# Performance work log

Hardware: AMD Instinct MI355X
Metric: run time of the kernel (lower is better)

## Reference

```python
import jax, jax.numpy as jnp
import numpy as np

N_NODES = 50000
N_EDGES = 800000
D_IN = 128
D_HID = 128
D_OUT = 128


def gcn_conv(x, W, b, src, dst, n_nodes):
    """PyG GCNConv: sym-normalized A+I aggregation, then bias.
    messages flow src -> dst; self-loops handled analytically."""
    h = x @ W  # [N, F_out]
    ones = jnp.ones(src.shape[0], dtype=h.dtype)
    deg = jax.ops.segment_sum(ones, dst, num_segments=n_nodes) + 1.0  # +1 self-loop
    dinv = jax.lax.rsqrt(deg)  # deg^-1/2
    norm = dinv[src] * dinv[dst]  # [E]
    agg = jax.ops.segment_sum(h[src] * norm[:, None], dst, num_segments=n_nodes)
    out = agg + h * (dinv * dinv)[:, None]  # self-loop term: dinv[i]^2 * h[i]
    return out + b


def setup_inputs() -> dict:
    key = jax.random.key(0)
    ks = jax.random.split(key, 12)
    x = jax.random.normal(ks[0], (N_NODES, D_IN), dtype=jnp.float32)
    edge_index = jax.random.randint(ks[1], (2, N_EDGES), 0, N_NODES, dtype=jnp.int64)

    def lin(k, fi, fo):
        s = 1.0 / np.sqrt(fi)
        return jax.random.uniform(k, (fi, fo), jnp.float32, -s, s)

    return {
        "x": x,
        "edge_index": edge_index,
        "W1": lin(ks[2], D_IN, D_HID), "b1": jnp.zeros((D_HID,), jnp.float32),
        "W2": lin(ks[3], D_HID, D_HID), "b2": jnp.zeros((D_HID,), jnp.float32),
        "W3": lin(ks[4], D_HID, D_OUT), "b3": jnp.zeros((D_OUT,), jnp.float32),
        "Wm1": lin(ks[5], 2 * D_HID, D_HID), "bm1": jnp.zeros((D_HID,), jnp.float32),
        "Wm2": lin(ks[6], D_HID, D_HID), "bm2": jnp.zeros((D_HID,), jnp.float32),
    }


def reference(x, edge_index, W1, b1, W2, b2, W3, b3, Wm1, bm1, Wm2, bm2):
    src, dst = edge_index[0], edge_index[1]
    n = x.shape[0]
    h = jax.nn.relu(gcn_conv(x, W1, b1, src, dst, n))
    h = jax.nn.relu(gcn_conv(h, W2, b2, src, dst, n))
    h = gcn_conv(h, W3, b3, src, dst, n)
    # edge head: gather node pairs, concat, 2-layer MLP
    ef = jnp.concatenate([h[src], h[dst]], axis=1)  # [E, 2*hidden]
    es = jax.nn.relu(ef @ Wm1 + bm1) @ Wm2 + bm2  # [E, hidden]
    return jnp.squeeze(es)
```

## Files before the change

kernel.cpp:

```cpp
#include <hip/hip_runtime.h>
#include <stdint.h>

typedef __attribute__((ext_vector_type(8))) short bf16x8;
typedef __attribute__((ext_vector_type(4))) float f32x4;

static __device__ __forceinline__ unsigned short f2b(float f) {
    unsigned int u = __float_as_uint(f);
    unsigned int r = u + 0x7fffu + ((u >> 16) & 1u);
    return (unsigned short)(r >> 16);
}
static __device__ __forceinline__ float b2f(unsigned short u) {
    return __uint_as_float((unsigned int)u << 16);
}
static __device__ __forceinline__ f32x4 b2f4(ushort4 u) {
    f32x4 r;
    r[0] = b2f(u.x); r[1] = b2f(u.y); r[2] = b2f(u.z); r[3] = b2f(u.w);
    return r;
}


__global__ void count_deg(const int* __restrict__ dst, int E, int* __restrict__ counts) {
    int e = blockIdx.x * 256 + threadIdx.x;
    if (e < E) atomicAdd(&counts[dst[e]], 1);
}

__global__ void scan_s1(const int* __restrict__ counts, int N,
                        int* __restrict__ rowstart, float* __restrict__ dinv,
                        int* __restrict__ psum) {
    __shared__ int wsum[16];
    int tid = threadIdx.x, wave = tid >> 6, lane = tid & 63;
    int i = blockIdx.x * 1024 + tid;
    int c = (i < N) ? counts[i] : 0;
    int x = c;
    #pragma unroll
    for (int off = 1; off < 64; off <<= 1) {
        int v = __shfl_up(x, off);
        if (lane >= off) x += v;
    }
    if (lane == 63) wsum[wave] = x;
    __syncthreads();
    int pre = 0, tot = 0;
    #pragma unroll
    for (int w = 0; w < 16; ++w) {
        int s = wsum[w];
        tot += s;
        if (w < wave) pre += s;
    }
    if (i < N) {
        rowstart[i] = pre + x - c;
        dinv[i] = rsqrtf((float)c + 1.0f);
    }
    if (tid == 0) psum[blockIdx.x] = tot;
}

__global__ void scan_s2(int* __restrict__ psum, int nchunk,
                        int* __restrict__ rowstart, int N) {
    __shared__ int wsum[16];
    int tid = threadIdx.x, wave = tid >> 6, lane = tid & 63;
    int v = (tid < nchunk) ? psum[tid] : 0;
    int x = v;
    #pragma unroll
    for (int off = 1; off < 64; off <<= 1) {
        int s = __shfl_up(x, off);
        if (lane >= off) x += s;
    }
    if (lane == 63) wsum[wave] = x;
    __syncthreads();
    int pre = 0, tot = 0;
    #pragma unroll
    for (int w = 0; w < 16; ++w) {
        int s = wsum[w];
        tot += s;
        if (w < wave) pre += s;
    }
    if (tid < nchunk) psum[tid] = pre + x - v;
    if (tid == 0) rowstart[N] = tot;
}

__global__ void scan_s3(int* __restrict__ rowstart, const int* __restrict__ psum,
                        int N, int* __restrict__ cursor) {
    int i = blockIdx.x * 1024 + threadIdx.x;
    if (i < N) {
        int r = rowstart[i] + psum[blockIdx.x];
        rowstart[i] = r;
        cursor[i] = r;
    }
}

__global__ void fill_csr(const int* __restrict__ src, const int* __restrict__ dst, int E,
                         int* __restrict__ cursor, int* __restrict__ csr_src,
                         int* __restrict__ csr_dst, int* __restrict__ csr_eid) {
    int e = blockIdx.x * 256 + threadIdx.x;
    if (e < E) {
        int d = dst[e];
        int p = atomicAdd(&cursor[d], 1);
        csr_src[p] = src[e];
        csr_dst[p] = d;
        csr_eid[p] = e;
    }
}


template <int IN_F32>
__global__ __launch_bounds__(256) void node_mfma(const void* __restrict__ inp,
                                                 const float* __restrict__ W,
                                                 unsigned short* __restrict__ outb, int N) {
    __shared__ __align__(16) unsigned short hl[64][136];
    int tid = threadIdx.x;
    int wid = tid >> 6, lane = tid & 63;
    int lg = lane >> 4, l15 = lane & 15;
    int tilebase = blockIdx.x * 64;

    bf16x8 a[2][4];
    #pragma unroll
    for (int mt = 0; mt < 2; ++mt) {
        int col = wid * 32 + mt * 16 + l15;
        #pragma unroll
        for (int kk = 0; kk < 4; ++kk) {
            bf16x8 af;
            #pragma unroll
            for (int ee = 0; ee < 8; ++ee)
                af[ee] = (short)f2b(W[(size_t)(kk * 32 + lg * 8 + ee) * 128 + col]);
            a[mt][kk] = af;
        }
    }

    #pragma unroll
    for (int p = 0; p < 4; ++p) {
        int idx = p * 256 + tid;
        int r = idx >> 4, ci = idx & 15;
        int row = tilebase + r;
        if (row >= N) row = N - 1;
        if (IN_F32) {
            const float* ip = (const float*)inp + (size_t)row * 128 + ci * 8;
            f32x4 x0 = *(const f32x4*)ip;
            f32x4 x1 = *(const f32x4*)(ip + 4);
            uint4 v;
            v.x = (unsigned int)f2b(x0[0]) | ((unsigned int)f2b(x0[1]) << 16);
            v.y = (unsigned int)f2b(x0[2]) | ((unsigned int)f2b(x0[3]) << 16);
            v.z = (unsigned int)f2b(x1[0]) | ((unsigned int)f2b(x1[1]) << 16);
            v.w = (unsigned int)f2b(x1[2]) | ((unsigned int)f2b(x1[3]) << 16);
            *(uint4*)&hl[r][ci * 8] = v;
        } else {
            *(uint4*)&hl[r][ci * 8] =
                *(const uint4*)((const unsigned short*)inp + (size_t)row * 128 + ci * 8);
        }
    }
    __syncthreads();

    f32x4 acc[2][4];
    #pragma unroll
    for (int mt = 0; mt < 2; ++mt)
        #pragma unroll
        for (int nt = 0; nt < 4; ++nt) acc[mt][nt] = (f32x4){0.f, 0.f, 0.f, 0.f};
    #pragma unroll
    for (int kk = 0; kk < 4; ++kk) {
        #pragma unroll
        for (int nt = 0; nt < 4; ++nt) {
            bf16x8 b = *(const bf16x8*)&hl[nt * 16 + l15][kk * 32 + lg * 8];
            acc[0][nt] = __builtin_amdgcn_mfma_f32_16x16x32_bf16(a[0][kk], b, acc[0][nt], 0, 0, 0);
            acc[1][nt] = __builtin_amdgcn_mfma_f32_16x16x32_bf16(a[1][kk], b, acc[1][nt], 0, 0, 0);
        }
    }
    #pragma unroll
    for (int mt = 0; mt < 2; ++mt) {
        int j = wid * 32 + mt * 16 + lg * 4;
        #pragma unroll
        for (int nt = 0; nt < 4; ++nt) {
            int node = tilebase + nt * 16 + l15;
            if (node < N) {
                unsigned int u0 = (unsigned int)f2b(acc[mt][nt][0]) | ((unsigned int)f2b(acc[mt][nt][1]) << 16);
                unsigned int u1 = (unsigned int)f2b(acc[mt][nt][2]) | ((unsigned int)f2b(acc[mt][nt][3]) << 16);
                *(uint2*)(outb + (size_t)node * 128 + j) = make_uint2(u0, u1);
            }
        }
    }
}


template <int RELU>
__global__ __launch_bounds__(256) void aggregate(
        const unsigned short* __restrict__ tb, const int* __restrict__ rowstart,
        const int* __restrict__ csr_src, const float* __restrict__ dinv,
        const float* __restrict__ bias, unsigned short* __restrict__ hb, int N) {
    int tid = threadIdx.x;
    int node = blockIdx.x * 8 + (tid >> 5);
    if (node >= N) return;
    int c = (tid & 31) * 4;
    float di = dinv[node];
    f32x4 self = b2f4(*(const ushort4*)(tb + (size_t)node * 128 + c));
    f32x4 acc = *(const f32x4*)(bias + c) + (di * di) * self;
    int rs = rowstart[node], re = rowstart[node + 1];
    int e = rs;
    for (; e + 3 < re; e += 4) {
        int s0 = csr_src[e], s1 = csr_src[e + 1];
        int s2 = csr_src[e + 2], s3 = csr_src[e + 3];
        float n0 = dinv[s0], n1 = dinv[s1], n2 = dinv[s2], n3 = dinv[s3];
        ushort4 r0 = *(const ushort4*)(tb + (size_t)s0 * 128 + c);
        ushort4 r1 = *(const ushort4*)(tb + (size_t)s1 * 128 + c);
        ushort4 r2 = *(const ushort4*)(tb + (size_t)s2 * 128 + c);
        ushort4 r3 = *(const ushort4*)(tb + (size_t)s3 * 128 + c);
        acc += (n0 * di) * b2f4(r0);
        acc += (n1 * di) * b2f4(r1);
        acc += (n2 * di) * b2f4(r2);
        acc += (n3 * di) * b2f4(r3);
    }
    for (; e < re; ++e) {
        int s0 = csr_src[e];
        acc += (dinv[s0] * di) * b2f4(*(const ushort4*)(tb + (size_t)s0 * 128 + c));
    }
    if (RELU) {
        #pragma unroll
        for (int j = 0; j < 4; ++j) acc[j] = fmaxf(acc[j], 0.f);
    }
    unsigned int u0 = (unsigned int)f2b(acc[0]) | ((unsigned int)f2b(acc[1]) << 16);
    unsigned int u1 = (unsigned int)f2b(acc[2]) | ((unsigned int)f2b(acc[3]) << 16);
    *(uint2*)(hb + (size_t)node * 128 + c) = make_uint2(u0, u1);
}


__global__ __launch_bounds__(256) void uv_gemm(const unsigned short* __restrict__ h3b,
                                               const float* __restrict__ Wm1,
                                               unsigned short* __restrict__ uvb, int N) {
    __shared__ __align__(16) unsigned short hl[64][136];
    int tid = threadIdx.x;
    int wid = tid >> 6, lane = tid & 63;
    int lg = lane >> 4, l15 = lane & 15;
    int tilebase = blockIdx.x * 64;

    bf16x8 a[4][4];
    #pragma unroll
    for (int mt = 0; mt < 4; ++mt) {
        int jc = wid * 64 + mt * 16 + l15;
        int koff = (jc >> 7) * 128;
        int col = jc & 127;
        #pragma unroll
        for (int kk = 0; kk < 4; ++kk) {
            bf16x8 af;
            #pragma unroll
            for (int ee = 0; ee < 8; ++ee)
                af[ee] = (short)f2b(Wm1[(size_t)(koff + kk * 32 + lg * 8 + ee) * 128 + col]);
            a[mt][kk] = af;
        }
    }

    #pragma unroll
    for (int p = 0; p < 4; ++p) {
        int idx = p * 256 + tid;
        int r = idx >> 4, ci = idx & 15;
        int row = tilebase + r;
        if (row >= N) row = N - 1;
        uint4 v = *(const uint4*)(h3b + (size_t)row * 128 + ci * 8);
        *(uint4*)&hl[r][ci * 8] = v;
    }
    __syncthreads();

    f32x4 acc[4][4];
    #pragma unroll
    for (int mt = 0; mt < 4; ++mt)
        #pragma unroll
        for (int nt = 0; nt < 4; ++nt) acc[mt][nt] = (f32x4){0.f, 0.f, 0.f, 0.f};
    #pragma unroll
    for (int kk = 0; kk < 4; ++kk) {
        #pragma unroll
        for (int nt = 0; nt < 4; ++nt) {
            bf16x8 b = *(const bf16x8*)&hl[nt * 16 + l15][kk * 32 + lg * 8];
            #pragma unroll
            for (int mt = 0; mt < 4; ++mt)
                acc[mt][nt] = __builtin_amdgcn_mfma_f32_16x16x32_bf16(a[mt][kk], b, acc[mt][nt], 0, 0, 0);
        }
    }
    #pragma unroll
    for (int mt = 0; mt < 4; ++mt) {
        int jc = wid * 64 + mt * 16 + lg * 4;
        #pragma unroll
        for (int nt = 0; nt < 4; ++nt) {
            int node = tilebase + nt * 16 + l15;
            if (node < N) {
                unsigned int u0 = (unsigned int)f2b(acc[mt][nt][0]) | ((unsigned int)f2b(acc[mt][nt][1]) << 16);
                unsigned int u1 = (unsigned int)f2b(acc[mt][nt][2]) | ((unsigned int)f2b(acc[mt][nt][3]) << 16);
                *(uint2*)(uvb + (size_t)node * 256 + jc) = make_uint2(u0, u1);
            }
        }
    }
}


__global__ __launch_bounds__(256, 4) void edge_head3(
        const unsigned short* __restrict__ uvb, const int* __restrict__ csr_src,
        const int* __restrict__ csr_dst, const int* __restrict__ csr_eid,
        const float* __restrict__ bm1, const float* __restrict__ Wm2,
        const float* __restrict__ bm2, float* __restrict__ out, int E, int ntiles) {
    __shared__ __align__(16) unsigned short zl[64][136];
    __shared__ int eid_l[64];
    int tid = threadIdx.x;
    int wid = tid >> 6, lane = tid & 63;
    int lg = lane >> 4, l15 = lane & 15;
    int es = tid >> 4;
    int ci = tid & 15;
    int c0 = ci * 8;

    bf16x8 a2[2][4];
    float b2v[2][4];
    #pragma unroll
    for (int mt = 0; mt < 2; ++mt) {
        int m = wid * 32 + mt * 16 + l15;
        #pragma unroll
        for (int kk = 0; kk < 4; ++kk) {
            bf16x8 af;
            #pragma unroll
            for (int ee = 0; ee < 8; ++ee)
                af[ee] = (short)f2b(Wm2[(size_t)(kk * 32 + lg * 8 + ee) * 128 + m]);
            a2[mt][kk] = af;
        }
        #pragma unroll
        for (int r = 0; r < 4; ++r)
            b2v[mt][r] = bm2[wid * 32 + mt * 16 + lg * 4 + r];
    }
    float bm1v[8];
    #pragma unroll
    for (int j = 0; j < 8; ++j) bm1v[j] = bm1[c0 + j];

    for (int tile = blockIdx.x; tile < ntiles; tile += gridDim.x) {
        __syncthreads();
        #pragma unroll
        for (int p = 0; p < 4; ++p) {
            int slot = tile * 64 + p * 16 + es;
            int cs = (slot < E) ? slot : (E - 1);
            int s = csr_src[cs], d = csr_dst[cs];
            if (ci == 0) eid_l[p * 16 + es] = (slot < E) ? csr_eid[cs] : -1;
            uint4 uu = *(const uint4*)(uvb + (size_t)s * 256 + c0);
            uint4 vv = *(const uint4*)(uvb + (size_t)d * 256 + 128 + c0);
            unsigned int w[4];
            {
                float z0 = fmaxf(b2f((unsigned short)(uu.x)) + b2f((unsigned short)(vv.x)) + bm1v[0], 0.f);
                float z1 = fmaxf(b2f((unsigned short)(uu.x >> 16)) + b2f((unsigned short)(vv.x >> 16)) + bm1v[1], 0.f);
                float z2 = fmaxf(b2f((unsigned short)(uu.y)) + b2f((unsigned short)(vv.y)) + bm1v[2], 0.f);
                float z3 = fmaxf(b2f((unsigned short)(uu.y >> 16)) + b2f((unsigned short)(vv.y >> 16)) + bm1v[3], 0.f);
                float z4 = fmaxf(b2f((unsigned short)(uu.z)) + b2f((unsigned short)(vv.z)) + bm1v[4], 0.f);
                float z5 = fmaxf(b2f((unsigned short)(uu.z >> 16)) + b2f((unsigned short)(vv.z >> 16)) + bm1v[5], 0.f);
                float z6 = fmaxf(b2f((unsigned short)(uu.w)) + b2f((unsigned short)(vv.w)) + bm1v[6], 0.f);
                float z7 = fmaxf(b2f((unsigned short)(uu.w >> 16)) + b2f((unsigned short)(vv.w >> 16)) + bm1v[7], 0.f);
                w[0] = (unsigned int)f2b(z0) | ((unsigned int)f2b(z1) << 16);
                w[1] = (unsigned int)f2b(z2) | ((unsigned int)f2b(z3) << 16);
                w[2] = (unsigned int)f2b(z4) | ((unsigned int)f2b(z5) << 16);
                w[3] = (unsigned int)f2b(z6) | ((unsigned int)f2b(z7) << 16);
            }
            *(uint4*)&zl[p * 16 + es][c0] = make_uint4(w[0], w[1], w[2], w[3]);
        }
        __syncthreads();

        f32x4 c2[2][4];
        #pragma unroll
        for (int mt = 0; mt < 2; ++mt)
            #pragma unroll
            for (int nt = 0; nt < 4; ++nt) c2[mt][nt] = (f32x4){0.f, 0.f, 0.f, 0.f};
        #pragma unroll
        for (int kk = 0; kk < 4; ++kk) {
            #pragma unroll
            for (int nt = 0; nt < 4; ++nt) {
                bf16x8 b = *(const bf16x8*)&zl[nt * 16 + l15][kk * 32 + lg * 8];
                c2[0][nt] = __builtin_amdgcn_mfma_f32_16x16x32_bf16(a2[0][kk], b, c2[0][nt], 0, 0, 0);
                c2[1][nt] = __builtin_amdgcn_mfma_f32_16x16x32_bf16(a2[1][kk], b, c2[1][nt], 0, 0, 0);
            }
        }
        #pragma unroll
        for (int mt = 0; mt < 2; ++mt) {
            #pragma unroll
            for (int nt = 0; nt < 4; ++nt) {
                int eg = eid_l[nt * 16 + l15];
                if (eg >= 0) {
                    f32x4 o;
                    #pragma unroll
                    for (int r = 0; r < 4; ++r) o[r] = c2[mt][nt][r] + b2v[mt][r];
                    *(f32x4*)(out + (size_t)eg * 128 + wid * 32 + mt * 16 + lg * 4) = o;
                }
            }
        }
    }
}


extern "C" void kernel_launch(void* const* d_in, const int* in_sizes, int n_in,
                              void* d_out, int out_size, void* d_ws, size_t ws_size,
                              hipStream_t stream) {
    const float* x  = (const float*)d_in[0];
    const int*   ei = (const int*)d_in[1];
    const float* W1 = (const float*)d_in[2];
    const float* b1 = (const float*)d_in[3];
    const float* W2 = (const float*)d_in[4];
    const float* b2 = (const float*)d_in[5];
    const float* W3 = (const float*)d_in[6];
    const float* b3 = (const float*)d_in[7];
    const float* Wm1 = (const float*)d_in[8];
    const float* bm1 = (const float*)d_in[9];
    const float* Wm2 = (const float*)d_in[10];
    const float* bm2 = (const float*)d_in[11];
    float* out = (float*)d_out;

    const int N = in_sizes[0] / 128;
    const int E = in_sizes[1] / 2;
    const int* src = ei;
    const int* dstp = ei + E;

    uintptr_t base = (uintptr_t)d_ws;
    auto alloc = [&](size_t bytes) -> void* {
        uintptr_t p = base;
        base += (bytes + 255) & ~(uintptr_t)255;
        return (void*)p;
    };
    int*   counts   = (int*)alloc((size_t)(N + 1) * 4);
    int*   rowstart = (int*)alloc((size_t)(N + 1) * 4);
    int*   cursor   = (int*)alloc((size_t)N * 4);
    float* dinv     = (float*)alloc((size_t)N * 4);
    int*   psum     = (int*)alloc(4096);
    int*   csr_s    = (int*)alloc((size_t)E * 4);
    int*   csr_d    = (int*)alloc((size_t)E * 4);
    int*   csr_e    = (int*)alloc((size_t)E * 4);
    unsigned short* tb  = (unsigned short*)alloc((size_t)N * 128 * 2);
    unsigned short* hb  = (unsigned short*)alloc((size_t)N * 128 * 2);
    unsigned short* uvb = (unsigned short*)alloc((size_t)N * 256 * 2);
    (void)ws_size; (void)n_in; (void)out_size;

    hipMemsetAsync(counts, 0, (size_t)(N + 1) * 4, stream);

    int egrid = (E + 255) / 256;
    int nchunk = (N + 1023) / 1024;
    count_deg<<<egrid, 256, 0, stream>>>(dstp, E, counts);
    scan_s1<<<nchunk, 1024, 0, stream>>>(counts, N, rowstart, dinv, psum);
    scan_s2<<<1, 1024, 0, stream>>>(psum, nchunk, rowstart, N);
    scan_s3<<<nchunk, 1024, 0, stream>>>(rowstart, psum, N, cursor);
    fill_csr<<<egrid, 256, 0, stream>>>(src, dstp, E, cursor, csr_s, csr_d, csr_e);

    int ggrid = (N + 63) / 64;
    int agrid = (N + 7) / 8;
    node_mfma<1><<<ggrid, 256, 0, stream>>>(x, W1, tb, N);
    aggregate<1><<<agrid, 256, 0, stream>>>(tb, rowstart, csr_s, dinv, b1, hb, N);
    node_mfma<0><<<ggrid, 256, 0, stream>>>(hb, W2, tb, N);
    aggregate<1><<<agrid, 256, 0, stream>>>(tb, rowstart, csr_s, dinv, b2, hb, N);
    node_mfma<0><<<ggrid, 256, 0, stream>>>(hb, W3, tb, N);
    aggregate<0><<<agrid, 256, 0, stream>>>(tb, rowstart, csr_s, dinv, b3, hb, N);

    uv_gemm<<<ggrid, 256, 0, stream>>>(hb, Wm1, uvb, N);

    int ntiles = (E + 63) / 64;
    int hgrid = ntiles < 2048 ? ntiles : 2048;
    edge_head3<<<hgrid, 256, 0, stream>>>(uvb, csr_s, csr_d, csr_e, bm1, Wm2, bm2, out, E, ntiles);
}
```

Baseline: 431.2 us.

## Precompute edge norms into CSR and software-pipeline edge head gathers

The CSR fill now stores each edge's symmetric normalization next to its source index as an int2. This removes the random dinv gather from all three aggregation passes, and the aggregation loop is unrolled to 8 edges. The edge head kernel prefetches the next tile's source-row gathers and indices into registers while the current tile's MFMA runs. Its grid and occupancy are also reduced to 768 blocks at 3 waves per SIMD. The cost is more register pressure and fewer resident blocks in the edge head.

```diff
diff --git a/kernel.cpp b/kernel.cpp
--- a/kernel.cpp
+++ b/kernel.cpp
@@ -88,13 +88,15 @@
 }
 
 __global__ void fill_csr(const int* __restrict__ src, const int* __restrict__ dst, int E,
-                         int* __restrict__ cursor, int* __restrict__ csr_src,
-                         int* __restrict__ csr_dst, int* __restrict__ csr_eid) {
+                         int* __restrict__ cursor, const float* __restrict__ dinv,
+                         int2* __restrict__ csr_sn, int* __restrict__ csr_dst,
+                         int* __restrict__ csr_eid) {
     int e = blockIdx.x * 256 + threadIdx.x;
     if (e < E) {
-        int d = dst[e];
+        int d = dst[e], s = src[e];
         int p = atomicAdd(&cursor[d], 1);
-        csr_src[p] = src[e];
+        float nrm = dinv[s] * dinv[d];
+        csr_sn[p] = make_int2(s, __float_as_int(nrm));
         csr_dst[p] = d;
         csr_eid[p] = e;
     }
@@ -181,7 +183,7 @@
 template <int RELU>
 __global__ __launch_bounds__(256) void aggregate(
         const unsigned short* __restrict__ tb, const int* __restrict__ rowstart,
-        const int* __restrict__ csr_src, const float* __restrict__ dinv,
+        const int2* __restrict__ csr_sn, const float* __restrict__ dinv,
         const float* __restrict__ bias, unsigned short* __restrict__ hb, int N) {
     int tid = threadIdx.x;
     int node = blockIdx.x * 8 + (tid >> 5);
@@ -190,24 +192,41 @@
     float di = dinv[node];
     f32x4 self = b2f4(*(const ushort4*)(tb + (size_t)node * 128 + c));
     f32x4 acc = *(const f32x4*)(bias + c) + (di * di) * self;
-    int rs = rowstart[node], re = rowstart[node + 1];
-    int e = rs;
+    int e = rowstart[node], re = rowstart[node + 1];
+    for (; e + 7 < re; e += 8) {
+        int2 p0 = csr_sn[e + 0], p1 = csr_sn[e + 1], p2 = csr_sn[e + 2], p3 = csr_sn[e + 3];
+        int2 p4 = csr_sn[e + 4], p5 = csr_sn[e + 5], p6 = csr_sn[e + 6], p7 = csr_sn[e + 7];
+        ushort4 r0 = *(const ushort4*)(tb + (size_t)p0.x * 128 + c);
+        ushort4 r1 = *(const ushort4*)(tb + (size_t)p1.x * 128 + c);
+        ushort4 r2 = *(const ushort4*)(tb + (size_t)p2.x * 128 + c);
+        ushort4 r3 = *(const ushort4*)(tb + (size_t)p3.x * 128 + c);
+        ushort4 r4 = *(const ushort4*)(tb + (size_t)p4.x * 128 + c);
+        ushort4 r5 = *(const ushort4*)(tb + (size_t)p5.x * 128 + c);
+        ushort4 r6 = *(const ushort4*)(tb + (size_t)p6.x * 128 + c);
+        ushort4 r7 = *(const ushort4*)(tb + (size_t)p7.x * 128 + c);
+        acc += __int_as_float(p0.y) * b2f4(r0);
+        acc += __int_as_float(p1.y) * b2f4(r1);
+        acc += __int_as_float(p2.y) * b2f4(r2);
+        acc += __int_as_float(p3.y) * b2f4(r3);
+        acc += __int_as_float(p4.y) * b2f4(r4);
+        acc += __int_as_float(p5.y) * b2f4(r5);
+        acc += __int_as_float(p6.y) * b2f4(r6);
+        acc += __int_as_float(p7.y) * b2f4(r7);
+    }
     for (; e + 3 < re; e += 4) {
-        int s0 = csr_src[e], s1 = csr_src[e + 1];
-        int s2 = csr_src[e + 2], s3 = csr_src[e + 3];
-        float n0 = dinv[s0], n1 = dinv[s1], n2 = dinv[s2], n3 = dinv[s3];
-        ushort4 r0 = *(const ushort4*)(tb + (size_t)s0 * 128 + c);
-        ushort4 r1 = *(const ushort4*)(tb + (size_t)s1 * 128 + c);
-        ushort4 r2 = *(const ushort4*)(tb + (size_t)s2 * 128 + c);
-        ushort4 r3 = *(const ushort4*)(tb + (size_t)s3 * 128 + c);
-        acc += (n0 * di) * b2f4(r0);
-        acc += (n1 * di) * b2f4(r1);
-        acc += (n2 * di) * b2f4(r2);
-        acc += (n3 * di) * b2f4(r3);
+        int2 p0 = csr_sn[e + 0], p1 = csr_sn[e + 1], p2 = csr_sn[e + 2], p3 = csr_sn[e + 3];
+        ushort4 r0 = *(const ushort4*)(tb + (size_t)p0.x * 128 + c);
+        ushort4 r1 = *(const ushort4*)(tb + (size_t)p1.x * 128 + c);
+        ushort4 r2 = *(const ushort4*)(tb + (size_t)p2.x * 128 + c);
+        ushort4 r3 = *(const ushort4*)(tb + (size_t)p3.x * 128 + c);
+        acc += __int_as_float(p0.y) * b2f4(r0);
+        acc += __int_as_float(p1.y) * b2f4(r1);
+        acc += __int_as_float(p2.y) * b2f4(r2);
+        acc += __int_as_float(p3.y) * b2f4(r3);
     }
     for (; e < re; ++e) {
-        int s0 = csr_src[e];
-        acc += (dinv[s0] * di) * b2f4(*(const ushort4*)(tb + (size_t)s0 * 128 + c));
+        int2 p0 = csr_sn[e];
+        acc += __int_as_float(p0.y) * b2f4(*(const ushort4*)(tb + (size_t)p0.x * 128 + c));
     }
     if (RELU) {
         #pragma unroll
@@ -286,8 +305,8 @@
 }
 
 
-__global__ __launch_bounds__(256, 4) void edge_head3(
-        const unsigned short* __restrict__ uvb, const int* __restrict__ csr_src,
+__global__ __launch_bounds__(256, 3) void edge_head4(
+        const unsigned short* __restrict__ uvb, const int2* __restrict__ csr_sn,
         const int* __restrict__ csr_dst, const int* __restrict__ csr_eid,
         const float* __restrict__ bm1, const float* __restrict__ Wm2,
         const float* __restrict__ bm2, float* __restrict__ out, int E, int ntiles) {
@@ -321,33 +340,48 @@
     #pragma unroll
     for (int j = 0; j < 8; ++j) bm1v[j] = bm1[c0 + j];
 
-    for (int tile = blockIdx.x; tile < ntiles; tile += gridDim.x) {
-        __syncthreads();
+    uint4 uuA[4], uuB[4];
+    int dA[4], dB[4], eidA[4], eidB[4];
+
+    auto stage = [&](int tile, uint4 (&uu)[4], int (&dd)[4], int (&ee)[4]) {
         #pragma unroll
         for (int p = 0; p < 4; ++p) {
             int slot = tile * 64 + p * 16 + es;
             int cs = (slot < E) ? slot : (E - 1);
-            int s = csr_src[cs], d = csr_dst[cs];
-            if (ci == 0) eid_l[p * 16 + es] = (slot < E) ? csr_eid[cs] : -1;
-            uint4 uu = *(const uint4*)(uvb + (size_t)s * 256 + c0);
-            uint4 vv = *(const uint4*)(uvb + (size_t)d * 256 + 128 + c0);
-            unsigned int w[4];
-            {
-                float z0 = fmaxf(b2f((unsigned short)(uu.x)) + b2f((unsigned short)(vv.x)) + bm1v[0], 0.f);
-                float z1 = fmaxf(b2f((unsigned short)(uu.x >> 16)) + b2f((unsigned short)(vv.x >> 16)) + bm1v[1], 0.f);
-                float z2 = fmaxf(b2f((unsigned short)(uu.y)) + b2f((unsigned short)(vv.y)) + bm1v[2], 0.f);
-                float z3 = fmaxf(b2f((unsigned short)(uu.y >> 16)) + b2f((unsigned short)(vv.y >> 16)) + bm1v[3], 0.f);
-                float z4 = fmaxf(b2f((unsigned short)(uu.z)) + b2f((unsigned short)(vv.z)) + bm1v[4], 0.f);
-                float z5 = fmaxf(b2f((unsigned short)(uu.z >> 16)) + b2f((unsigned short)(vv.z >> 16)) + bm1v[5], 0.f);
-                float z6 = fmaxf(b2f((unsigned short)(uu.w)) + b2f((unsigned short)(vv.w)) + bm1v[6], 0.f);
-                float z7 = fmaxf(b2f((unsigned short)(uu.w >> 16)) + b2f((unsigned short)(vv.w >> 16)) + bm1v[7], 0.f);
-                w[0] = (unsigned int)f2b(z0) | ((unsigned int)f2b(z1) << 16);
-                w[1] = (unsigned int)f2b(z2) | ((unsigned int)f2b(z3) << 16);
-                w[2] = (unsigned int)f2b(z4) | ((unsigned int)f2b(z5) << 16);
-                w[3] = (unsigned int)f2b(z6) | ((unsigned int)f2b(z7) << 16);
-            }
-            *(uint4*)&zl[p * 16 + es][c0] = make_uint4(w[0], w[1], w[2], w[3]);
-        }
+            int s = csr_sn[cs].x;
+            dd[p] = csr_dst[cs];
+            ee[p] = (slot < E) ? csr_eid[cs] : -1;
+            uu[p] = *(const uint4*)(uvb + (size_t)s * 256 + c0);
+        }
+    };
+
+    int t = blockIdx.x;
+    if (t < ntiles) stage(t, uuA, dA, eidA);
+    for (; t < ntiles; t += gridDim.x) {
+        __syncthreads();
+        #pragma unroll
+        for (int p = 0; p < 4; ++p) {
+            uint4 vv = *(const uint4*)(uvb + (size_t)dA[p] * 256 + 128 + c0);
+            uint4 uu = uuA[p];
+            float z0 = fmaxf(b2f((unsigned short)(uu.x)) + b2f((unsigned short)(vv.x)) + bm1v[0], 0.f);
+            float z1 = fmaxf(b2f((unsigned short)(uu.x >> 16)) + b2f((unsigned short)(vv.x >> 16)) + bm1v[1], 0.f);
+            float z2 = fmaxf(b2f((unsigned short)(uu.y)) + b2f((unsigned short)(vv.y)) + bm1v[2], 0.f);
+            float z3 = fmaxf(b2f((unsigned short)(uu.y >> 16)) + b2f((unsigned short)(vv.y >> 16)) + bm1v[3], 0.f);
+            float z4 = fmaxf(b2f((unsigned short)(uu.z)) + b2f((unsigned short)(vv.z)) + bm1v[4], 0.f);
+            float z5 = fmaxf(b2f((unsigned short)(uu.z >> 16)) + b2f((unsigned short)(vv.z >> 16)) + bm1v[5], 0.f);
+            float z6 = fmaxf(b2f((unsigned short)(uu.w)) + b2f((unsigned short)(vv.w)) + bm1v[6], 0.f);
+            float z7 = fmaxf(b2f((unsigned short)(uu.w >> 16)) + b2f((unsigned short)(vv.w >> 16)) + bm1v[7], 0.f);
+            uint4 w;
+            w.x = (unsigned int)f2b(z0) | ((unsigned int)f2b(z1) << 16);
+            w.y = (unsigned int)f2b(z2) | ((unsigned int)f2b(z3) << 16);
+            w.z = (unsigned int)f2b(z4) | ((unsigned int)f2b(z5) << 16);
+            w.w = (unsigned int)f2b(z6) | ((unsigned int)f2b(z7) << 16);
+            *(uint4*)&zl[p * 16 + es][c0] = w;
+            if (ci == 0) eid_l[p * 16 + es] = eidA[p];
+        }
+        int tn = t + gridDim.x;
+        bool more = (tn < ntiles);
+        if (more) stage(tn, uuB, dB, eidB);
         __syncthreads();
 
         f32x4 c2[2][4];
@@ -375,6 +409,12 @@
                     for (int r = 0; r < 4; ++r) o[r] = c2[mt][nt][r] + b2v[mt][r];
                     *(f32x4*)(out + (size_t)eg * 128 + wid * 32 + mt * 16 + lg * 4) = o;
                 }
+            }
+        }
+        if (more) {
+            #pragma unroll
+            for (int p = 0; p < 4; ++p) {
+                uuA[p] = uuB[p]; dA[p] = dB[p]; eidA[p] = eidB[p];
             }
         }
     }
@@ -414,7 +454,7 @@
     int*   cursor   = (int*)alloc((size_t)N * 4);
     float* dinv     = (float*)alloc((size_t)N * 4);
     int*   psum     = (int*)alloc(4096);
-    int*   csr_s    = (int*)alloc((size_t)E * 4);
+    int2*  csr_sn   = (int2*)alloc((size_t)E * 8);
     int*   csr_d    = (int*)alloc((size_t)E * 4);
     int*   csr_e    = (int*)alloc((size_t)E * 4);
     unsigned short* tb  = (unsigned short*)alloc((size_t)N * 128 * 2);
@@ -430,20 +470,20 @@
     scan_s1<<<nchunk, 1024, 0, stream>>>(counts, N, rowstart, dinv, psum);
     scan_s2<<<1, 1024, 0, stream>>>(psum, nchunk, rowstart, N);
     scan_s3<<<nchunk, 1024, 0, stream>>>(rowstart, psum, N, cursor);
-    fill_csr<<<egrid, 256, 0, stream>>>(src, dstp, E, cursor, csr_s, csr_d, csr_e);
+    fill_csr<<<egrid, 256, 0, stream>>>(src, dstp, E, cursor, dinv, csr_sn, csr_d, csr_e);
 
     int ggrid = (N + 63) / 64;
     int agrid = (N + 7) / 8;
     node_mfma<1><<<ggrid, 256, 0, stream>>>(x, W1, tb, N);
-    aggregate<1><<<agrid, 256, 0, stream>>>(tb, rowstart, csr_s, dinv, b1, hb, N);
+    aggregate<1><<<agrid, 256, 0, stream>>>(tb, rowstart, csr_sn, dinv, b1, hb, N);
     node_mfma<0><<<ggrid, 256, 0, stream>>>(hb, W2, tb, N);
-    aggregate<1><<<agrid, 256, 0, stream>>>(tb, rowstart, csr_s, dinv, b2, hb, N);
+    aggregate<1><<<agrid, 256, 0, stream>>>(tb, rowstart, csr_sn, dinv, b2, hb, N);
     node_mfma<0><<<ggrid, 256, 0, stream>>>(hb, W3, tb, N);
-    aggregate<0><<<agrid, 256, 0, stream>>>(tb, rowstart, csr_s, dinv, b3, hb, N);
+    aggregate<0><<<agrid, 256, 0, stream>>>(tb, rowstart, csr_sn, dinv, b3, hb, N);
 
     uv_gemm<<<ggrid, 256, 0, stream>>>(hb, Wm1, uvb, N);
 
     int ntiles = (E + 63) / 64;
-    int hgrid = ntiles < 2048 ? ntiles : 2048;
-    edge_head3<<<hgrid, 256, 0, stream>>>(uvb, csr_s, csr_d, csr_e, bm1, Wm2, bm2, out, E, ntiles);
-}
+    int hgrid = ntiles < 768 ? ntiles : 768;
+    edge_head4<<<hgrid, 256, 0, stream>>>(uvb, csr_sn, csr_d, csr_e, bm1, Wm2, bm2, out, E, ntiles);
+}
```

New measurement: 427.4 us. No clear change (-0.9%).
